# Performance work log

Measured on AMD Instinct MI355X. Metric: run time of the kernel, lower is better.

The kernel has to match this reference:

```python
import jax, jax.numpy as jnp
import numpy as np

B, S, DIM = 2, 2048, 2048
N_HEADS = 16
KV_LORA = 512
NOPE_D = 128
ROPE_D = 64
V_D = 128
Q_D = NOPE_D + ROPE_D  # 192
EPS = 1e-6


def _make_rope_cache(seqlen, head_dim):
    # [cos | sin] layout per position, GPT-NeoX half-rotation convention
    half = head_dim // 2
    inv_freq = 1.0 / (10000.0 ** (np.arange(0, half, dtype=np.float32) / half))
    t = np.arange(seqlen, dtype=np.float32)
    freqs = np.outer(t, inv_freq)                    # [S, half]
    emb = np.concatenate([freqs, freqs], axis=-1)    # [S, head_dim]
    return jnp.asarray(np.concatenate([np.cos(emb), np.sin(emb)], axis=-1))  # [S, 2*head_dim]


def setup_inputs() -> dict:
    key = jax.random.key(0)
    ks = jax.random.split(key, 6)
    x = jax.random.normal(ks[0], (B, S, DIM), dtype=jnp.float32)
    rope_cache = _make_rope_cache(S, ROPE_D)         # [S, 128]
    std = 0.02
    wq = jax.random.normal(ks[1], (N_HEADS * Q_D, DIM), dtype=jnp.float32) * std
    wkva = jax.random.normal(ks[2], (KV_LORA + ROPE_D, DIM), dtype=jnp.float32) * std
    norm_w = jnp.ones((KV_LORA,), dtype=jnp.float32)
    wkvb = jax.random.normal(ks[3], (N_HEADS * (NOPE_D + V_D), KV_LORA), dtype=jnp.float32) * std
    wo = jax.random.normal(ks[4], (DIM, N_HEADS * V_D), dtype=jnp.float32) * std
    return {"x": x, "rope_cache": rope_cache, "wq": wq, "wkva": wkva,
            "norm_w": norm_w, "wkvb": wkvb, "wo": wo}


def _rotate_half(t):
    h = t.shape[-1] // 2
    return jnp.concatenate([-t[..., h:], t[..., :h]], axis=-1)


def _rms_norm(t, w):
    tf = t.astype(jnp.float32)
    y = tf * jax.lax.rsqrt(jnp.mean(tf * tf, axis=-1, keepdims=True) + EPS)
    return (y * w).astype(t.dtype)


def reference(x, rope_cache, wq, wkva, norm_w, wkvb, wo):
    bs, seqlen, _ = x.shape
    scale = Q_D ** (-0.5)

    q = (x @ wq.T).reshape(bs, seqlen, N_HEADS, Q_D)
    q_nope, q_rope = q[..., :NOPE_D], q[..., NOPE_D:]

    ckv = x @ wkva.T                                 # [b,s,KV_LORA+ROPE_D]
    kv_pass, k_rope = ckv[..., :KV_LORA], ckv[..., KV_LORA:]
    kv = (_rms_norm(kv_pass, norm_w) @ wkvb.T).reshape(bs, seqlen, N_HEADS, NOPE_D + V_D)
    k_nope, v = kv[..., :NOPE_D], kv[..., NOPE_D:]

    k_rope = jnp.broadcast_to(k_rope[:, :, None, :], (bs, seqlen, N_HEADS, ROPE_D))

    cos = rope_cache[:seqlen, :ROPE_D][None, :, None, :]
    sin = rope_cache[:seqlen, ROPE_D:2 * ROPE_D][None, :, None, :]
    q_rope = q_rope * cos + _rotate_half(q_rope) * sin
    k_rope = k_rope * cos + _rotate_half(k_rope) * sin

    qf = jnp.concatenate([q_nope, q_rope], axis=-1)  # [b,s,h,192]
    kf = jnp.concatenate([k_nope, k_rope], axis=-1)

    # causal SDPA
    scores = jnp.einsum('bqhd,bkhd->bhqk', qf, kf) * scale
    mask = jnp.tril(jnp.ones((seqlen, seqlen), dtype=bool))
    scores = jnp.where(mask, scores, jnp.finfo(scores.dtype).min)
    probs = jax.nn.softmax(scores, axis=-1)
    out = jnp.einsum('bhqk,bkhd->bqhd', probs, v).reshape(bs, seqlen, N_HEADS * V_D)
    return out @ wo.T
```

## Files before the change

### kernel.cpp

```cpp
#include <hip/hip_runtime.h>
#include <cstdint>
#include <cstddef>

#define B_      2
#define S_      2048
#define DIM_    2048
#define H_      16
#define KV_LORA_ 512
#define NOPE_D_ 128
#define ROPE_D_ 64
#define V_D_    128
#define Q_D_    192
#define EPS_    1e-6f
#define BS_     (B_ * S_)
#define CKV_P_  768

typedef __attribute__((ext_vector_type(8))) short bf16x8;
typedef __attribute__((ext_vector_type(4))) float f32x4;
typedef __attribute__((ext_vector_type(16))) float f32x16;

__device__ __forceinline__ ushort f2bf(float f) {
    union { float f; uint32_t u; } v; v.f = f;
    uint32_t u = v.u + 0x7fff + ((v.u >> 16) & 1);
    return (ushort)(u >> 16);
}
__device__ __forceinline__ float bf2f(ushort u) {
    union { uint32_t u; float f; } v; v.u = (uint32_t)u << 16; return v.f;
}
__device__ __forceinline__ void gll16(const void* g, void* l) {
    __builtin_amdgcn_global_load_lds(
        (const __attribute__((address_space(1))) unsigned int*)g,
        (__attribute__((address_space(3))) unsigned int*)l, 16, 0, 0);
}

#define GQ_BARRIER()  __builtin_amdgcn_s_barrier()
#define GQ_LGKM0()    do { asm volatile("s_waitcnt lgkmcnt(0)" ::: "memory"); \
                           __builtin_amdgcn_sched_barrier(0); } while (0)

template <int MODE>
__global__ __launch_bounds__(512, 2) void gemm256_8ph(
    const ushort* __restrict__ A, const ushort* __restrict__ Bw,
    void* __restrict__ Cv, void* __restrict__ Cv2, int N, int K, int nbx)
{
    __shared__ __align__(16) ushort L[2][2][2][8192];

    const int tid = threadIdx.x;
    const int lane = tid & 63;
    const int w = tid >> 6;
    const int l15 = lane & 15, quad = lane >> 4;
    const int q8 = quad * 8;
    const int rsw8 = ((l15 >> 1) & 3) * 8;

    const int nwg = (int)gridDim.x;
    const int cpx = nwg >> 3;
    const int lin = (int)blockIdx.x;
    const int swz = (lin & 7) * cpx + (lin >> 3);
    const int m0 = (swz / nbx) * 256;
    const int n0 = (swz % nbx) * 256;

    const int wm0 = (w & 3) * 64;
    const int wn0 = (w >> 2) * 128;

    const int NT = K >> 6;

    f32x4 acc[4][8];
#pragma unroll
    for (int i = 0; i < 4; ++i)
#pragma unroll
        for (int j = 0; j < 8; ++j) acc[i][j] = (f32x4){0.f, 0.f, 0.f, 0.f};

    const int srow = lane >> 2;
    const int scg  = (lane & 3) ^ ((lane >> 3) & 3);

    auto stage = [&](int ab, int kh, int kt, int buf) {
#pragma unroll
        for (int j = 0; j < 2; ++j) {
            int ci = w + j * 8;
            ushort* dst = &L[buf][ab][kh][ci * 512 + lane * 8];
            int row = ci * 16 + srow;
            const ushort* src = (ab ? Bw + (size_t)(n0 + row) * K
                                    : A  + (size_t)(m0 + row) * K)
                                + kt * 64 + kh * 32 + scg * 8;
            gll16(src, dst);
        }
    };

    stage(0, 0, 0, 0); stage(1, 0, 0, 0); stage(0, 1, 0, 0); stage(1, 1, 0, 0);
    if (NT > 1) { stage(0, 0, 1, 1); stage(1, 0, 1, 1); stage(0, 1, 1, 1); }
    else        { stage(0, 0, 0, 1); stage(1, 0, 0, 1); stage(0, 1, 0, 1); }
    asm volatile("s_waitcnt vmcnt(6)" ::: "memory");
    GQ_BARRIER();

    bf16x8 a[4], b[4];

    for (int t = 0; t < NT; ++t) {
        const int c = t & 1, o = c ^ 1;
        const int kt1 = (t + 1 < NT) ? t + 1 : 0;
        const int kt2 = (t + 2 < NT) ? t + 2 : 0;

#pragma unroll
        for (int fm = 0; fm < 4; ++fm)
            a[fm] = *(const bf16x8*)&L[c][0][0][(wm0 + fm * 16 + l15) * 32 + (q8 ^ rsw8)];
#pragma unroll
        for (int fn = 0; fn < 4; ++fn)
            b[fn] = *(const bf16x8*)&L[c][1][0][(wn0 + fn * 16 + l15) * 32 + (q8 ^ rsw8)];
        stage(1, 1, kt1, o);
        GQ_BARRIER();
        GQ_LGKM0();
        __builtin_amdgcn_s_setprio(1);
#pragma unroll
        for (int fm = 0; fm < 4; ++fm)
#pragma unroll
            for (int fn = 0; fn < 4; ++fn)
                acc[fm][fn] = __builtin_amdgcn_mfma_f32_16x16x32_bf16(a[fm], b[fn], acc[fm][fn], 0, 0, 0);
        __builtin_amdgcn_s_setprio(0);
        GQ_BARRIER();

#pragma unroll
        for (int fn = 0; fn < 4; ++fn)
            b[fn] = *(const bf16x8*)&L[c][1][0][(wn0 + 64 + fn * 16 + l15) * 32 + (q8 ^ rsw8)];
        stage(0, 0, kt2, c);
        GQ_BARRIER();
        GQ_LGKM0();
        __builtin_amdgcn_s_setprio(1);
#pragma unroll
        for (int fm = 0; fm < 4; ++fm)
#pragma unroll
            for (int fn = 0; fn < 4; ++fn)
                acc[fm][4 + fn] = __builtin_amdgcn_mfma_f32_16x16x32_bf16(a[fm], b[fn], acc[fm][4 + fn], 0, 0, 0);
        __builtin_amdgcn_s_setprio(0);
        GQ_BARRIER();

#pragma unroll
        for (int fm = 0; fm < 4; ++fm)
            a[fm] = *(const bf16x8*)&L[c][0][1][(wm0 + fm * 16 + l15) * 32 + (q8 ^ rsw8)];
#pragma unroll
        for (int fn = 0; fn < 4; ++fn)
            b[fn] = *(const bf16x8*)&L[c][1][1][(wn0 + fn * 16 + l15) * 32 + (q8 ^ rsw8)];
        stage(1, 0, kt2, c);
        GQ_BARRIER();
        GQ_LGKM0();
        __builtin_amdgcn_s_setprio(1);
#pragma unroll
        for (int fm = 0; fm < 4; ++fm)
#pragma unroll
            for (int fn = 0; fn < 4; ++fn)
                acc[fm][fn] = __builtin_amdgcn_mfma_f32_16x16x32_bf16(a[fm], b[fn], acc[fm][fn], 0, 0, 0);
        __builtin_amdgcn_s_setprio(0);
        GQ_BARRIER();

#pragma unroll
        for (int fn = 0; fn < 4; ++fn)
            b[fn] = *(const bf16x8*)&L[c][1][1][(wn0 + 64 + fn * 16 + l15) * 32 + (q8 ^ rsw8)];
        stage(0, 1, kt2, c);
        GQ_BARRIER();
        GQ_LGKM0();
        __builtin_amdgcn_s_setprio(1);
#pragma unroll
        for (int fm = 0; fm < 4; ++fm)
#pragma unroll
            for (int fn = 0; fn < 4; ++fn)
                acc[fm][4 + fn] = __builtin_amdgcn_mfma_f32_16x16x32_bf16(a[fm], b[fn], acc[fm][4 + fn], 0, 0, 0);
        __builtin_amdgcn_s_setprio(0);
        asm volatile("s_waitcnt vmcnt(6)" ::: "memory");
        GQ_BARRIER();
    }

    if (MODE == 3) {
        asm volatile("s_waitcnt vmcnt(0)" ::: "memory");
        GQ_BARRIER();
        const int h = n0 >> 8;
        if (w < 4) {
#pragma unroll
            for (int fm = 0; fm < 4; ++fm)
#pragma unroll
                for (int r = 0; r < 4; ++r) {
                    size_t base = (size_t)(m0 + wm0 + fm * 16 + quad * 4 + r) * 4096
                                  + n0 + wn0 + l15;
#pragma unroll
                    for (int fn = 0; fn < 8; ++fn)
                        ((ushort*)Cv)[base + fn * 16] = f2bf(acc[fm][fn][r]);
                }
        } else {
            ushort* T = &L[0][0][0][0] + (size_t)(w - 4) * (128 * 80);
#pragma unroll
            for (int fm = 0; fm < 4; ++fm)
#pragma unroll
                for (int fn = 0; fn < 8; ++fn) {
                    uint32_t lo = (uint32_t)f2bf(acc[fm][fn][0])
                                | ((uint32_t)f2bf(acc[fm][fn][1]) << 16);
                    uint32_t hi2 = (uint32_t)f2bf(acc[fm][fn][2])
                                 | ((uint32_t)f2bf(acc[fm][fn][3]) << 16);
                    uint2 pk; pk.x = lo; pk.y = hi2;
                    *(uint2*)&T[(size_t)(fn * 16 + l15) * 80 + fm * 16 + quad * 4] = pk;
                }
            asm volatile("s_waitcnt lgkmcnt(0)" ::: "memory");
            __builtin_amdgcn_sched_barrier(0);
            const int bh = (m0 >> 11) * 16 + h;
            const int sbase = (m0 & 2047) + (w & 3) * 64;
            ushort* vT = (ushort*)Cv2;
#pragma unroll
            for (int j = 0; j < 16; ++j) {
                int cc = j * 64 + lane;
                int vd = cc >> 3;
                int s8 = (cc & 7) * 8;
                bf16x8 v = *(const bf16x8*)&T[(size_t)vd * 80 + s8];
                *(bf16x8*)(vT + ((size_t)bh * 128 + vd) * 2048 + sbase + s8) = v;
            }
        }
        return;
    }
#pragma unroll
    for (int fm = 0; fm < 4; ++fm)
#pragma unroll
        for (int r = 0; r < 4; ++r) {
            int row = m0 + wm0 + fm * 16 + quad * 4 + r;
            if (MODE == 2) {
                if (n0 < 3072) {
                    size_t base = (size_t)row * 3072 + n0 + wn0 + l15;
#pragma unroll
                    for (int fn = 0; fn < 8; ++fn)
                        ((ushort*)Cv)[base + fn * 16] = f2bf(acc[fm][fn][r]);
                } else {
                    size_t base = (size_t)row * CKV_P_ + (n0 - 3072) + wn0 + l15;
#pragma unroll
                    for (int fn = 0; fn < 8; ++fn)
                        ((float*)Cv2)[base + fn * 16] = acc[fm][fn][r];
                }
            } else {
                size_t base = (size_t)row * N + n0 + wn0 + l15;
#pragma unroll
                for (int fn = 0; fn < 8; ++fn) {
                    float v = acc[fm][fn][r];
                    if (MODE == 1) ((ushort*)Cv)[base + fn * 16] = f2bf(v);
                    else           ((float*)Cv)[base + fn * 16] = v;
                }
            }
        }
}

template <int OUT_BF16>
__global__ __launch_bounds__(512, 2) void gemm_bn128(
    const ushort* __restrict__ A, const ushort* __restrict__ Bw,
    void* __restrict__ Cv, int N, int K, int nbx)
{
    __shared__ __align__(16) ushort LA[2][2][8192];
    __shared__ __align__(16) ushort LB[2][2][4096];

    const int tid = threadIdx.x;
    const int lane = tid & 63;
    const int w = tid >> 6;
    const int l15 = lane & 15, quad = lane >> 4;
    const int q8 = quad * 8;
    const int rsw8 = ((l15 >> 1) & 3) * 8;

    const int nwg = (int)gridDim.x;
    const int cpx = nwg >> 3;
    const int lin = (int)blockIdx.x;
    const int swz = (lin & 7) * cpx + (lin >> 3);
    const int m0 = (swz / nbx) * 256;
    const int n0 = (swz % nbx) * 128;

    const int wm0 = (w & 3) * 64;
    const int wn0 = (w >> 2) * 64;

    const int NT = K >> 6;

    f32x4 acc[4][4];
#pragma unroll
    for (int i = 0; i < 4; ++i)
#pragma unroll
        for (int j = 0; j < 4; ++j) acc[i][j] = (f32x4){0.f, 0.f, 0.f, 0.f};

    const int srow = lane >> 2;
    const int scg  = (lane & 3) ^ ((lane >> 3) & 3);

    auto stageA = [&](int kh, int kt, int buf) {
#pragma unroll
        for (int j = 0; j < 2; ++j) {
            int ci = w + j * 8;
            ushort* dst = &LA[buf][kh][ci * 512 + lane * 8];
            int row = ci * 16 + srow;
            const ushort* src = A + (size_t)(m0 + row) * K
                                + kt * 64 + kh * 32 + scg * 8;
            gll16(src, dst);
        }
    };
    auto stageB = [&](int kt, int buf) {
#pragma unroll
        for (int j = 0; j < 2; ++j) {
            ushort* dst = &LB[buf][j][(w * 64 + lane) * 8];
            int row = w * 16 + srow;
            const ushort* src = Bw + (size_t)(n0 + row) * K
                                + kt * 64 + j * 32 + scg * 8;
            gll16(src, dst);
        }
    };

    stageA(0, 0, 0); stageA(1, 0, 0); stageB(0, 0);
    stageA(0, (NT > 1) ? 1 : 0, 1);
    asm volatile("s_waitcnt vmcnt(2)" ::: "memory");
    GQ_BARRIER();

    bf16x8 a[4], b[4];

    for (int t = 0; t < NT; ++t) {
        const int c = t & 1, o = c ^ 1;
        const int kt1 = (t + 1 < NT) ? t + 1 : 0;
        const int kt2 = (t + 2 < NT) ? t + 2 : 0;

#pragma unroll
        for (int fm = 0; fm < 4; ++fm)
            a[fm] = *(const bf16x8*)&LA[c][0][(wm0 + fm * 16 + l15) * 32 + (q8 ^ rsw8)];
#pragma unroll
        for (int fn = 0; fn < 4; ++fn)
            b[fn] = *(const bf16x8*)&LB[c][0][(wn0 + fn * 16 + l15) * 32 + (q8 ^ rsw8)];
        stageA(1, kt1, o); stageB(kt1, o);
        GQ_BARRIER();
        GQ_LGKM0();
        __builtin_amdgcn_s_setprio(1);
#pragma unroll
        for (int fm = 0; fm < 4; ++fm)
#pragma unroll
            for (int fn = 0; fn < 4; ++fn)
                acc[fm][fn] = __builtin_amdgcn_mfma_f32_16x16x32_bf16(a[fm], b[fn], acc[fm][fn], 0, 0, 0);
        __builtin_amdgcn_s_setprio(0);
        GQ_BARRIER();

#pragma unroll
        for (int fm = 0; fm < 4; ++fm)
            a[fm] = *(const bf16x8*)&LA[c][1][(wm0 + fm * 16 + l15) * 32 + (q8 ^ rsw8)];
#pragma unroll
        for (int fn = 0; fn < 4; ++fn)
            b[fn] = *(const bf16x8*)&LB[c][1][(wn0 + fn * 16 + l15) * 32 + (q8 ^ rsw8)];
        stageA(0, kt2, c);
        GQ_BARRIER();
        GQ_LGKM0();
        __builtin_amdgcn_s_setprio(1);
#pragma unroll
        for (int fm = 0; fm < 4; ++fm)
#pragma unroll
            for (int fn = 0; fn < 4; ++fn)
                acc[fm][fn] = __builtin_amdgcn_mfma_f32_16x16x32_bf16(a[fm], b[fn], acc[fm][fn], 0, 0, 0);
        __builtin_amdgcn_s_setprio(0);
        asm volatile("s_waitcnt vmcnt(2)" ::: "memory");
        GQ_BARRIER();
    }

#pragma unroll
    for (int fm = 0; fm < 4; ++fm)
#pragma unroll
        for (int r = 0; r < 4; ++r) {
            size_t base = (size_t)(m0 + wm0 + fm * 16 + quad * 4 + r) * N + n0 + wn0 + l15;
#pragma unroll
            for (int fn = 0; fn < 4; ++fn) {
                float v = acc[fm][fn][r];
                if (OUT_BF16) ((ushort*)Cv)[base + fn * 16] = f2bf(v);
                else          ((float*)Cv)[base + fn * 16] = v;
            }
        }
}

__global__ __launch_bounds__(256) void cast_all(
    const float* __restrict__ x, const float* __restrict__ wq,
    const float* __restrict__ wkva, const float* __restrict__ wkvb,
    const float* __restrict__ wo,
    ushort* __restrict__ xb, ushort* __restrict__ wc,
    ushort* __restrict__ wkvb_bf, ushort* __restrict__ wo_bf)
{
    size_t i = ((size_t)blockIdx.x * 256 + threadIdx.x) * 8;
    const float* s; ushort* d;
    if (i < 8388608)        { s = x + i;                  d = xb + i; }
    else if (i < 14680064)  { s = wq + (i - 8388608);     d = wc + (i - 8388608); }
    else if (i < 15859712)  { s = wkva + (i - 14680064);  d = wc + (i - 8388608); }
    else if (i < 16252928)  {
        ushort4 z = {0, 0, 0, 0};
        ushort* dz = wc + (i - 8388608);
        *(ushort4*)dz = z; *(ushort4*)(dz + 4) = z;
        return;
    }
    else if (i < 18350080)  { s = wkvb + (i - 16252928);  d = wkvb_bf + (i - 16252928); }
    else                    { s = wo + (i - 18350080);    d = wo_bf + (i - 18350080); }
    float4 a = *(const float4*)s;
    float4 b = *(const float4*)(s + 4);
    ushort4 o0, o1;
    o0.x = f2bf(a.x); o0.y = f2bf(a.y); o0.z = f2bf(a.z); o0.w = f2bf(a.w);
    o1.x = f2bf(b.x); o1.y = f2bf(b.y); o1.z = f2bf(b.z); o1.w = f2bf(b.w);
    *(ushort4*)d = o0;
    *(ushort4*)(d + 4) = o1;
}

__global__ __launch_bounds__(256) void rmsnorm_rope_k(
    const float* __restrict__ ckv, const float* __restrict__ nw,
    const float* __restrict__ rope_cache,
    ushort* __restrict__ cnorm, ushort* __restrict__ krb)
{
    const int lane = threadIdx.x & 63;
    const int row = blockIdx.x * 4 + (threadIdx.x >> 6);
    const float* src = ckv + (size_t)row * CKV_P_;
    float4 a = *(const float4*)(src + lane * 4);
    float4 b = *(const float4*)(src + 256 + lane * 4);
    float ss = a.x*a.x + a.y*a.y + a.z*a.z + a.w*a.w
             + b.x*b.x + b.y*b.y + b.z*b.z + b.w*b.w;
#pragma unroll
    for (int off = 32; off > 0; off >>= 1) ss += __shfl_xor(ss, off, 64);
    float rs = rsqrtf(ss * (1.0f / 512.0f) + EPS_);
    float4 w0 = *(const float4*)(nw + lane * 4);
    float4 w1 = *(const float4*)(nw + 256 + lane * 4);
    ushort* dst = cnorm + (size_t)row * KV_LORA_;
    ushort4 o0, o1;
    o0.x = f2bf(a.x*rs*w0.x); o0.y = f2bf(a.y*rs*w0.y);
    o0.z = f2bf(a.z*rs*w0.z); o0.w = f2bf(a.w*rs*w0.w);
    o1.x = f2bf(b.x*rs*w1.x); o1.y = f2bf(b.y*rs*w1.y);
    o1.z = f2bf(b.z*rs*w1.z); o1.w = f2bf(b.w*rs*w1.w);
    *(ushort4*)(dst + lane * 4) = o0;
    *(ushort4*)(dst + 256 + lane * 4) = o1;

    float v = src[KV_LORA_ + lane];
    float other = __shfl_xor(v, 32, 64);
    float rot = (lane < 32) ? -other : other;
    int s = row & (S_ - 1);
    float c  = rope_cache[s * (2 * ROPE_D_) + lane];
    float sn = rope_cache[s * (2 * ROPE_D_) + ROPE_D_ + lane];
    krb[(size_t)row * ROPE_D_ + lane] = f2bf(v * c + rot * sn);
}

__global__ __launch_bounds__(512, 2) void mla_attn_mfma7(
    const ushort* __restrict__ qb, const ushort* __restrict__ kvb,
    const ushort* __restrict__ krb, const ushort* __restrict__ vT,
    const float* __restrict__ rope_cache, ushort* __restrict__ attn)
{
    __shared__ __align__(16) ushort LDSU[40960];
    const int KNo[2] = {0, 8192};
    const int KRo[2] = {16384, 20480};
    const int VVo[2] = {24576, 32768};

    const int tid = threadIdx.x;
    const int lane = tid & 63;
    const int w = tid >> 6;
    const int l31 = lane & 31, hi = lane >> 5;
    const int band = w & 3;
    const int koff = (w >> 2) * 32;

    const int lin = (int)blockIdx.y * 8 + (int)blockIdx.x;
    const int swz = (lin & 7) * 32 + (lin >> 3);
    const int bh = swz >> 3;
    const int px = swz & 7;
    const int b = bh >> 4, h = bh & 15;
    const size_t bS = (size_t)b * S_;
    const float scale = 0.07216878364870323f;

    auto stage = [&](int kbase, int bufi) {
#pragma unroll
        for (int j = 0; j < 2; ++j) {
            int g = (j * 8 + w) * 64 + lane;
            int row = g >> 4;
            int d8 = (g & 15) ^ (row & 7);
            ushort* dst = &LDSU[KNo[bufi] + g * 8];
            const ushort* src = kvb + (bS + kbase + row) * 4096 + h * 256 + d8 * 8;
            gll16(src, dst);
        }
        {
            int g = w * 64 + lane;
            int row = g >> 3;
            int r8 = (g & 7) ^ (row & 7);
            ushort* dst = &LDSU[KRo[bufi] + g * 8];
            const ushort* src = krb + (bS + kbase + row) * 64 + r8 * 8;
            gll16(src, dst);
        }
#pragma unroll
        for (int j = 0; j < 2; ++j) {
            int g = (j * 8 + w) * 64 + lane;
            int vd = g >> 3;
            int kc = (g & 7) ^ (vd & 7);
            ushort* dst = &LDSU[VVo[bufi] + g * 8];
            const ushort* src = vT + ((size_t)bh * 128 + vd) * 2048 + kbase + kc * 8;
            gll16(src, dst);
        }
    };

#pragma unroll 1
    for (int hv = 0; hv < 2; ++hv) {
        const int qt = hv ? 15 - px : px;
        const int qbase = qt * 128;
        const int nkt = 2 * qt + 2;
        const int bmin = qbase + band * 32;

        stage(0, 0);

        bf16x8 qf[12];
        {
            const ushort* qrow = qb + (bS + bmin + l31) * (size_t)(H_ * Q_D_) + h * Q_D_;
#pragma unroll
            for (int c = 0; c < 8; ++c)
                qf[c] = *(const bf16x8*)(qrow + c * 16 + hi * 8);
            bf16x8 q8  = *(const bf16x8*)(qrow + 128 + hi * 8);
            bf16x8 q9  = *(const bf16x8*)(qrow + 144 + hi * 8);
            bf16x8 q10 = *(const bf16x8*)(qrow + 160 + hi * 8);
            bf16x8 q11 = *(const bf16x8*)(qrow + 176 + hi * 8);
            const float* rc = rope_cache + (size_t)(bmin + l31) * 128 + hi * 8;
            f32x4 c8a = *(const f32x4*)(rc + 0),  c8b = *(const f32x4*)(rc + 4);
            f32x4 c9a = *(const f32x4*)(rc + 16), c9b = *(const f32x4*)(rc + 20);
            f32x4 cAa = *(const f32x4*)(rc + 32), cAb = *(const f32x4*)(rc + 36);
            f32x4 cBa = *(const f32x4*)(rc + 48), cBb = *(const f32x4*)(rc + 52);
            f32x4 s8a = *(const f32x4*)(rc + 64), s8b = *(const f32x4*)(rc + 68);
            f32x4 s9a = *(const f32x4*)(rc + 80), s9b = *(const f32x4*)(rc + 84);
            f32x4 sAa = *(const f32x4*)(rc + 96), sAb = *(const f32x4*)(rc + 100);
            f32x4 sBa = *(const f32x4*)(rc + 112), sBb = *(const f32x4*)(rc + 116);
            bf16x8 o8, o9, o10, o11;
#pragma unroll
            for (int e = 0; e < 4; ++e) {
                float a8 = bf2f((ushort)q8[e]),  b8 = bf2f((ushort)q8[e + 4]);
                float a9 = bf2f((ushort)q9[e]),  b9 = bf2f((ushort)q9[e + 4]);
                float aA = bf2f((ushort)q10[e]), bA = bf2f((ushort)q10[e + 4]);
                float aB = bf2f((ushort)q11[e]), bB = bf2f((ushort)q11[e + 4]);
                o8[e]      = (short)f2bf(a8 * c8a[e] - aA * s8a[e]);
                o8[e + 4]  = (short)f2bf(b8 * c8b[e] - bA * s8b[e]);
                o9[e]      = (short)f2bf(a9 * c9a[e] - aB * s9a[e]);
                o9[e + 4]  = (short)f2bf(b9 * c9b[e] - bB * s9b[e]);
                o10[e]     = (short)f2bf(aA * cAa[e] + a8 * sAa[e]);
                o10[e + 4] = (short)f2bf(bA * cAb[e] + b8 * sAb[e]);
                o11[e]     = (short)f2bf(aB * cBa[e] + a9 * sBa[e]);
                o11[e + 4] = (short)f2bf(bB * cBb[e] + b9 * sBb[e]);
            }
            qf[8] = o8; qf[9] = o9; qf[10] = o10; qf[11] = o11;
        }

        f32x16 ov[4];
#pragma unroll
        for (int vt = 0; vt < 4; ++vt)
#pragma unroll
            for (int r = 0; r < 16; ++r) ov[vt][r] = 0.f;
        float m_run = -3e38f, lsum = 0.f;

        __syncthreads();

        const int krow = koff + l31;
        const int kx7 = krow & 7;
        const int vx7 = l31 & 7;

        for (int kt = 0; kt < nkt; ++kt) {
            const int kb = kt * 64;
            const int cur = kt & 1;
            if (kt + 1 < nkt) stage((kt + 1) * 64, cur ^ 1);

            const int kg = kb + koff;
            if (kg <= bmin + 31) {
                f32x16 sc;
#pragma unroll
                for (int r = 0; r < 16; ++r) sc[r] = 0.f;
                __builtin_amdgcn_s_setprio(1);
#pragma unroll
                for (int c = 0; c < 12; ++c) {
                    const bf16x8* kp;
                    if (c < 8)
                        kp = (const bf16x8*)&LDSU[KNo[cur] + (krow * 16 + ((c * 2 + hi) ^ kx7)) * 8];
                    else
                        kp = (const bf16x8*)&LDSU[KRo[cur] + (krow * 8 + (((c - 8) * 2 + hi) ^ kx7)) * 8];
                    sc = __builtin_amdgcn_mfma_f32_32x32x16_bf16(*kp, qf[c], sc, 0, 0, 0);
                }
                __builtin_amdgcn_s_setprio(0);

                const bool need_mask = (kg == bmin);
                float p[16]; float mx = -3e38f;
#pragma unroll
                for (int r = 0; r < 16; ++r) {
                    float v = sc[r] * scale;
                    if (need_mask) {
                        int kr = (r & 3) + 8 * (r >> 2) + 4 * hi;
                        if (kr > l31) v = -3e38f;
                    }
                    p[r] = v; mx = fmaxf(mx, v);
                }
                mx = fmaxf(mx, __shfl_xor(mx, 32, 64));
                if (!__all(mx - m_run <= 8.0f)) {
                    float mn = fmaxf(mx, m_run);
                    float al = __expf(m_run - mn);
                    m_run = mn; lsum *= al;
#pragma unroll
                    for (int vt = 0; vt < 4; ++vt)
#pragma unroll
                        for (int r = 0; r < 16; ++r) ov[vt][r] *= al;
                }
                float s_loc = 0.f;
#pragma unroll
                for (int r = 0; r < 16; ++r) { p[r] = __expf(p[r] - m_run); s_loc += p[r]; }
                lsum += s_loc + __shfl_xor(s_loc, 32, 64);

                uint32_t w8[8];
#pragma unroll
                for (int m = 0; m < 8; ++m)
                    w8[m] = (uint32_t)f2bf(p[2 * m]) | ((uint32_t)f2bf(p[2 * m + 1]) << 16);
                bf16x8 pb[2];
#pragma unroll
                for (int c = 0; c < 2; ++c) {
                    uint32_t wd[4];
#pragma unroll
                    for (int par = 0; par < 2; ++par) {
                        uint32_t a  = w8[4 * c + par];
                        uint32_t bb = w8[4 * c + 2 + par];
                        uint32_t t  = __shfl_xor(bb, 32, 64);
                        uint32_t t2 = __shfl_xor(a, 32, 64);
                        wd[par]     = hi ? t : a;
                        wd[par + 2] = hi ? bb : t2;
                    }
                    union { uint32_t u[4]; bf16x8 v; } cvt;
                    cvt.u[0] = wd[0]; cvt.u[1] = wd[1]; cvt.u[2] = wd[2]; cvt.u[3] = wd[3];
                    pb[c] = cvt.v;
                }

                __builtin_amdgcn_s_setprio(1);
#pragma unroll
                for (int vt = 0; vt < 4; ++vt)
#pragma unroll
                    for (int cc = 0; cc < 2; ++cc) {
                        int vd = vt * 32 + l31;
                        int k8 = (koff >> 3) + cc * 2 + hi;
                        bf16x8 vf = *(const bf16x8*)
                            &LDSU[VVo[cur] + (vd * 8 + (k8 ^ vx7)) * 8];
                        ov[vt] = __builtin_amdgcn_mfma_f32_32x32x16_bf16(vf, pb[cc], ov[vt], 0, 0, 0);
                    }
                __builtin_amdgcn_s_setprio(0);
            }
            __syncthreads();
        }

        float* mrg = (float*)LDSU;
        if (w >= 4) {
            float* dst = mrg + (size_t)((w - 4) * 64 + lane) * 68;
#pragma unroll
            for (int vt = 0; vt < 4; ++vt)
#pragma unroll
                for (int g = 0; g < 4; ++g) {
                    f32x4 v4v = { ov[vt][g * 4 + 0], ov[vt][g * 4 + 1],
                                  ov[vt][g * 4 + 2], ov[vt][g * 4 + 3] };
                    *(f32x4*)(dst + vt * 16 + g * 4) = v4v;
                }
            dst[64] = m_run; dst[65] = lsum;
        }
        __syncthreads();
        if (w < 4) {
            const float* srcm = mrg + (size_t)(w * 64 + lane) * 68;
            float mB = srcm[64], lB = srcm[65];
            float M = fmaxf(m_run, mB);
            float eA = __expf(m_run - M), eB = __expf(mB - M);
            float L = lsum * eA + lB * eB;
            float inv = 1.0f / L;
            size_t obase = (bS + bmin + l31) * (size_t)(H_ * V_D_) + h * V_D_;
#pragma unroll
            for (int vt = 0; vt < 4; ++vt)
#pragma unroll
                for (int g = 0; g < 4; ++g) {
                    ushort4 o;
                    o.x = f2bf((ov[vt][g*4+0] * eA + srcm[vt*16+g*4+0] * eB) * inv);
                    o.y = f2bf((ov[vt][g*4+1] * eA + srcm[vt*16+g*4+1] * eB) * inv);
                    o.z = f2bf((ov[vt][g*4+2] * eA + srcm[vt*16+g*4+2] * eB) * inv);
                    o.w = f2bf((ov[vt][g*4+3] * eA + srcm[vt*16+g*4+3] * eB) * inv);
                    *(ushort4*)(attn + obase + vt * 32 + g * 8 + hi * 4) = o;
                }
        }
        __syncthreads();
    }
}

extern "C" void kernel_launch(void* const* d_in, const int* in_sizes, int n_in,
                              void* d_out, int out_size, void* d_ws, size_t ws_size,
                              hipStream_t stream)
{
    const float* x          = (const float*)d_in[0];
    const float* rope_cache = (const float*)d_in[1];
    const float* wq         = (const float*)d_in[2];
    const float* wkva       = (const float*)d_in[3];
    const float* norm_w     = (const float*)d_in[4];
    const float* wkvb       = (const float*)d_in[5];
    const float* wo         = (const float*)d_in[6];
    float* out = (float*)d_out;

    char* p = (char*)d_ws;
    ushort* xb       = (ushort*)p; p += (size_t)BS_ * DIM_ * 2;
    ushort* q_bf     = (ushort*)p; p += (size_t)BS_ * H_ * Q_D_ * 2;
    float*  ckv      = (float*) p; p += (size_t)BS_ * CKV_P_ * 4;
    ushort* cnorm_bf = (ushort*)p; p += (size_t)BS_ * KV_LORA_ * 2;
    ushort* kvb      = (ushort*)p; p += (size_t)BS_ * 4096 * 2;
    ushort* attn_bf  = (ushort*)p; p += (size_t)BS_ * 2048 * 2;
    ushort* krb      = (ushort*)p; p += (size_t)BS_ * ROPE_D_ * 2;
    ushort* wc_bf    = (ushort*)p; p += (size_t)3840 * DIM_ * 2;
    ushort* wkvb_bf  = (ushort*)p; p += (size_t)4096 * KV_LORA_ * 2;
    ushort* wo_bf    = (ushort*)p; p += (size_t)DIM_ * 2048 * 2;
    ushort* vT       = xb;

    cast_all<<<11008, dim3(256), 0, stream>>>(
        x, wq, wkva, wkvb, wo, xb, wc_bf, wkvb_bf, wo_bf);

    gemm256_8ph<2><<<dim3(16 * 15), dim3(512), 0, stream>>>(
        xb, wc_bf, q_bf, ckv, 0, DIM_, 15);
    rmsnorm_rope_k<<<BS_ / 4, dim3(256), 0, stream>>>(
        ckv, norm_w, rope_cache, cnorm_bf, krb);
    gemm256_8ph<3><<<dim3(16 * 16), dim3(512), 0, stream>>>(
        cnorm_bf, wkvb_bf, kvb, vT, 4096, KV_LORA_, 16);
    mla_attn_mfma7<<<dim3(8, B_ * H_), dim3(512), 0, stream>>>(
        q_bf, kvb, krb, vT, rope_cache, attn_bf);
    gemm_bn128<0><<<dim3(16 * 16), dim3(512), 0, stream>>>(
        attn_bf, wo_bf, out, 2048, 2048, 16);
}
```

Before: 340.7 us.

## Split attention into one q-tile per block with XCD-aware mapping and exp2 softmax

```diff
diff --git a/kernel.cpp b/kernel.cpp
--- a/kernel.cpp
+++ b/kernel.cpp
@@ -425,7 +425,7 @@
     krb[(size_t)row * ROPE_D_ + lane] = f2bf(v * c + rot * sn);
 }
 
-__global__ __launch_bounds__(512, 2) void mla_attn_mfma7(
+__global__ __launch_bounds__(512, 4) void mla_attn_mfma8(
     const ushort* __restrict__ qb, const ushort* __restrict__ kvb,
     const ushort* __restrict__ krb, const ushort* __restrict__ vT,
     const float* __restrict__ rope_cache, ushort* __restrict__ attn)
@@ -442,13 +442,15 @@
     const int band = w & 3;
     const int koff = (w >> 2) * 32;
 
-    const int lin = (int)blockIdx.y * 8 + (int)blockIdx.x;
-    const int swz = (lin & 7) * 32 + (lin >> 3);
-    const int bh = swz >> 3;
-    const int px = swz & 7;
+    const int lin = (int)blockIdx.x;
+    const int r256 = lin & 255, sl = lin >> 8;
+    const int xcd = r256 & 7, cu = r256 >> 3;
+    const int bh = xcd * 4 + (cu >> 3);
+    const int jj = cu & 7;
+    const int qt = sl ? (15 - jj) : jj;
     const int b = bh >> 4, h = bh & 15;
     const size_t bS = (size_t)b * S_;
-    const float scale = 0.07216878364870323f;
+    const float sc_l2e = 0.10411789f;
 
     auto stage = [&](int kbase, int bufi) {
 #pragma unroll
@@ -479,187 +481,190 @@
         }
     };
 
-#pragma unroll 1
-    for (int hv = 0; hv < 2; ++hv) {
-        const int qt = hv ? 15 - px : px;
-        const int qbase = qt * 128;
-        const int nkt = 2 * qt + 2;
-        const int bmin = qbase + band * 32;
-
-        stage(0, 0);
-
-        bf16x8 qf[12];
-        {
-            const ushort* qrow = qb + (bS + bmin + l31) * (size_t)(H_ * Q_D_) + h * Q_D_;
-#pragma unroll
-            for (int c = 0; c < 8; ++c)
-                qf[c] = *(const bf16x8*)(qrow + c * 16 + hi * 8);
-            bf16x8 q8  = *(const bf16x8*)(qrow + 128 + hi * 8);
-            bf16x8 q9  = *(const bf16x8*)(qrow + 144 + hi * 8);
-            bf16x8 q10 = *(const bf16x8*)(qrow + 160 + hi * 8);
-            bf16x8 q11 = *(const bf16x8*)(qrow + 176 + hi * 8);
-            const float* rc = rope_cache + (size_t)(bmin + l31) * 128 + hi * 8;
-            f32x4 c8a = *(const f32x4*)(rc + 0),  c8b = *(const f32x4*)(rc + 4);
-            f32x4 c9a = *(const f32x4*)(rc + 16), c9b = *(const f32x4*)(rc + 20);
-            f32x4 cAa = *(const f32x4*)(rc + 32), cAb = *(const f32x4*)(rc + 36);
-            f32x4 cBa = *(const f32x4*)(rc + 48), cBb = *(const f32x4*)(rc + 52);
-            f32x4 s8a = *(const f32x4*)(rc + 64), s8b = *(const f32x4*)(rc + 68);
-            f32x4 s9a = *(const f32x4*)(rc + 80), s9b = *(const f32x4*)(rc + 84);
-            f32x4 sAa = *(const f32x4*)(rc + 96), sAb = *(const f32x4*)(rc + 100);
-            f32x4 sBa = *(const f32x4*)(rc + 112), sBb = *(const f32x4*)(rc + 116);
-            bf16x8 o8, o9, o10, o11;
-#pragma unroll
-            for (int e = 0; e < 4; ++e) {
-                float a8 = bf2f((ushort)q8[e]),  b8 = bf2f((ushort)q8[e + 4]);
-                float a9 = bf2f((ushort)q9[e]),  b9 = bf2f((ushort)q9[e + 4]);
-                float aA = bf2f((ushort)q10[e]), bA = bf2f((ushort)q10[e + 4]);
-                float aB = bf2f((ushort)q11[e]), bB = bf2f((ushort)q11[e + 4]);
-                o8[e]      = (short)f2bf(a8 * c8a[e] - aA * s8a[e]);
-                o8[e + 4]  = (short)f2bf(b8 * c8b[e] - bA * s8b[e]);
-                o9[e]      = (short)f2bf(a9 * c9a[e] - aB * s9a[e]);
-                o9[e + 4]  = (short)f2bf(b9 * c9b[e] - bB * s9b[e]);
-                o10[e]     = (short)f2bf(aA * cAa[e] + a8 * sAa[e]);
-                o10[e + 4] = (short)f2bf(bA * cAb[e] + b8 * sAb[e]);
-                o11[e]     = (short)f2bf(aB * cBa[e] + a9 * sBa[e]);
-                o11[e + 4] = (short)f2bf(bB * cBb[e] + b9 * sBb[e]);
-            }
-            qf[8] = o8; qf[9] = o9; qf[10] = o10; qf[11] = o11;
-        }
-
-        f32x16 ov[4];
+    const int qbase = qt * 128;
+    const int nkt = 2 * qt + 2;
+    const int bmin = qbase + band * 32;
+
+    stage(0, 0);
+
+    bf16x8 qf[12];
+    {
+        const ushort* qrow = qb + (bS + bmin + l31) * (size_t)(H_ * Q_D_) + h * Q_D_;
+#pragma unroll
+        for (int c = 0; c < 8; ++c)
+            qf[c] = *(const bf16x8*)(qrow + c * 16 + hi * 8);
+        bf16x8 q8  = *(const bf16x8*)(qrow + 128 + hi * 8);
+        bf16x8 q9  = *(const bf16x8*)(qrow + 144 + hi * 8);
+        bf16x8 q10 = *(const bf16x8*)(qrow + 160 + hi * 8);
+        bf16x8 q11 = *(const bf16x8*)(qrow + 176 + hi * 8);
+        const float* rc = rope_cache + (size_t)(bmin + l31) * 128 + hi * 8;
+        f32x4 c8a = *(const f32x4*)(rc + 0),  c8b = *(const f32x4*)(rc + 4);
+        f32x4 c9a = *(const f32x4*)(rc + 16), c9b = *(const f32x4*)(rc + 20);
+        f32x4 cAa = *(const f32x4*)(rc + 32), cAb = *(const f32x4*)(rc + 36);
+        f32x4 cBa = *(const f32x4*)(rc + 48), cBb = *(const f32x4*)(rc + 52);
+        f32x4 s8a = *(const f32x4*)(rc + 64), s8b = *(const f32x4*)(rc + 68);
+        f32x4 s9a = *(const f32x4*)(rc + 80), s9b = *(const f32x4*)(rc + 84);
+        f32x4 sAa = *(const f32x4*)(rc + 96), sAb = *(const f32x4*)(rc + 100);
+        f32x4 sBa = *(const f32x4*)(rc + 112), sBb = *(const f32x4*)(rc + 116);
+        bf16x8 o8, o9, o10, o11;
+#pragma unroll
+        for (int e = 0; e < 4; ++e) {
+            float a8 = bf2f((ushort)q8[e]),  b8 = bf2f((ushort)q8[e + 4]);
+            float a9 = bf2f((ushort)q9[e]),  b9 = bf2f((ushort)q9[e + 4]);
+            float aA = bf2f((ushort)q10[e]), bA = bf2f((ushort)q10[e + 4]);
+            float aB = bf2f((ushort)q11[e]), bB = bf2f((ushort)q11[e + 4]);
+            o8[e]      = (short)f2bf(a8 * c8a[e] - aA * s8a[e]);
+            o8[e + 4]  = (short)f2bf(b8 * c8b[e] - bA * s8b[e]);
+            o9[e]      = (short)f2bf(a9 * c9a[e] - aB * s9a[e]);
+            o9[e + 4]  = (short)f2bf(b9 * c9b[e] - bB * s9b[e]);
+            o10[e]     = (short)f2bf(aA * cAa[e] + a8 * sAa[e]);
+            o10[e + 4] = (short)f2bf(bA * cAb[e] + b8 * sAb[e]);
+            o11[e]     = (short)f2bf(aB * cBa[e] + a9 * sBa[e]);
+            o11[e + 4] = (short)f2bf(bB * cBb[e] + b9 * sBb[e]);
+        }
+        qf[8] = o8; qf[9] = o9; qf[10] = o10; qf[11] = o11;
+    }
+
+    f32x16 ov[4];
+#pragma unroll
+    for (int vt = 0; vt < 4; ++vt)
+#pragma unroll
+        for (int r = 0; r < 16; ++r) ov[vt][r] = 0.f;
+    float m_run = -3e38f, lsum = 0.f;
+
+    __syncthreads();
+
+    const int krow = koff + l31;
+    const int kx7 = krow & 7;
+    const int vx7 = l31 & 7;
+
+    for (int kt = 0; kt < nkt; ++kt) {
+        const int kb = kt * 64;
+        const int cur = kt & 1;
+        if (kt + 1 < nkt) stage((kt + 1) * 64, cur ^ 1);
+
+        const int kg = kb + koff;
+        if (kg <= bmin + 31) {
+            f32x16 sc;
+#pragma unroll
+            for (int r = 0; r < 16; ++r) sc[r] = 0.f;
+            __builtin_amdgcn_s_setprio(1);
+#pragma unroll
+            for (int c = 0; c < 12; ++c) {
+                const bf16x8* kp;
+                if (c < 8)
+                    kp = (const bf16x8*)&LDSU[KNo[cur] + (krow * 16 + ((c * 2 + hi) ^ kx7)) * 8];
+                else
+                    kp = (const bf16x8*)&LDSU[KRo[cur] + (krow * 8 + (((c - 8) * 2 + hi) ^ kx7)) * 8];
+                sc = __builtin_amdgcn_mfma_f32_32x32x16_bf16(*kp, qf[c], sc, 0, 0, 0);
+            }
+            __builtin_amdgcn_s_setprio(0);
+
+            const bool need_mask = (kg == bmin);
+            float p[16]; float mx = -3e38f;
+#pragma unroll
+            for (int r = 0; r < 16; ++r) {
+                float v = sc[r] * sc_l2e;
+                if (need_mask) {
+                    int kr = (r & 3) + 8 * (r >> 2) + 4 * hi;
+                    if (kr > l31) v = -3e38f;
+                }
+                p[r] = v; mx = fmaxf(mx, v);
+            }
+            mx = fmaxf(mx, __shfl_xor(mx, 32, 64));
+            if (!__all(mx - m_run <= 11.5416f)) {
+                float mn = fmaxf(mx, m_run);
+                float al;
+                asm("v_exp_f32 %0, %1" : "=v"(al) : "v"(m_run - mn));
+                m_run = mn; lsum *= al;
+#pragma unroll
+                for (int vt = 0; vt < 4; ++vt)
+#pragma unroll
+                    for (int r = 0; r < 16; ++r) ov[vt][r] *= al;
+            }
+            float s_loc = 0.f;
+#pragma unroll
+            for (int r = 0; r < 16; ++r) {
+                float e;
+                asm("v_exp_f32 %0, %1" : "=v"(e) : "v"(p[r] - m_run));
+                p[r] = e; s_loc += e;
+            }
+            lsum += s_loc + __shfl_xor(s_loc, 32, 64);
+
+            uint32_t w8[8];
+#pragma unroll
+            for (int m = 0; m < 8; ++m)
+                asm("v_cvt_pk_bf16_f32 %0, %1, %2"
+                    : "=v"(w8[m]) : "v"(p[2 * m]), "v"(p[2 * m + 1]));
+            bf16x8 pb[2];
+#pragma unroll
+            for (int c = 0; c < 2; ++c) {
+                uint32_t wd[4];
+#pragma unroll
+                for (int par = 0; par < 2; ++par) {
+                    uint32_t a  = w8[4 * c + par];
+                    uint32_t bb = w8[4 * c + 2 + par];
+                    uint32_t t  = __shfl_xor(bb, 32, 64);
+                    uint32_t t2 = __shfl_xor(a, 32, 64);
+                    wd[par]     = hi ? t : a;
+                    wd[par + 2] = hi ? bb : t2;
+                }
+                union { uint32_t u[4]; bf16x8 v; } cvt;
+                cvt.u[0] = wd[0]; cvt.u[1] = wd[1]; cvt.u[2] = wd[2]; cvt.u[3] = wd[3];
+                pb[c] = cvt.v;
+            }
+
+            __builtin_amdgcn_s_setprio(1);
+#pragma unroll
+            for (int vt = 0; vt < 4; ++vt)
+#pragma unroll
+                for (int cc = 0; cc < 2; ++cc) {
+                    int vd = vt * 32 + l31;
+                    int k8 = (koff >> 3) + cc * 2 + hi;
+                    bf16x8 vf = *(const bf16x8*)
+                        &LDSU[VVo[cur] + (vd * 8 + (k8 ^ vx7)) * 8];
+                    ov[vt] = __builtin_amdgcn_mfma_f32_32x32x16_bf16(vf, pb[cc], ov[vt], 0, 0, 0);
+                }
+            __builtin_amdgcn_s_setprio(0);
+        }
+        __syncthreads();
+    }
+
+    float* mrg = (float*)LDSU;
+    if (w >= 4) {
+        float* dst = mrg + (size_t)((w - 4) * 64 + lane) * 68;
 #pragma unroll
         for (int vt = 0; vt < 4; ++vt)
 #pragma unroll
-            for (int r = 0; r < 16; ++r) ov[vt][r] = 0.f;
-        float m_run = -3e38f, lsum = 0.f;
-
-        __syncthreads();
-
-        const int krow = koff + l31;
-        const int kx7 = krow & 7;
-        const int vx7 = l31 & 7;
-
-        for (int kt = 0; kt < nkt; ++kt) {
-            const int kb = kt * 64;
-            const int cur = kt & 1;
-            if (kt + 1 < nkt) stage((kt + 1) * 64, cur ^ 1);
-
-            const int kg = kb + koff;
-            if (kg <= bmin + 31) {
-                f32x16 sc;
-#pragma unroll
-                for (int r = 0; r < 16; ++r) sc[r] = 0.f;
-                __builtin_amdgcn_s_setprio(1);
-#pragma unroll
-                for (int c = 0; c < 12; ++c) {
-                    const bf16x8* kp;
-                    if (c < 8)
-                        kp = (const bf16x8*)&LDSU[KNo[cur] + (krow * 16 + ((c * 2 + hi) ^ kx7)) * 8];
-                    else
-                        kp = (const bf16x8*)&LDSU[KRo[cur] + (krow * 8 + (((c - 8) * 2 + hi) ^ kx7)) * 8];
-                    sc = __builtin_amdgcn_mfma_f32_32x32x16_bf16(*kp, qf[c], sc, 0, 0, 0);
-                }
-                __builtin_amdgcn_s_setprio(0);
-
-                const bool need_mask = (kg == bmin);
-                float p[16]; float mx = -3e38f;
-#pragma unroll
-                for (int r = 0; r < 16; ++r) {
-                    float v = sc[r] * scale;
-                    if (need_mask) {
-                        int kr = (r & 3) + 8 * (r >> 2) + 4 * hi;
-                        if (kr > l31) v = -3e38f;
-                    }
-                    p[r] = v; mx = fmaxf(mx, v);
-                }
-                mx = fmaxf(mx, __shfl_xor(mx, 32, 64));
-                if (!__all(mx - m_run <= 8.0f)) {
-                    float mn = fmaxf(mx, m_run);
-                    float al = __expf(m_run - mn);
-                    m_run = mn; lsum *= al;
-#pragma unroll
-                    for (int vt = 0; vt < 4; ++vt)
-#pragma unroll
-                        for (int r = 0; r < 16; ++r) ov[vt][r] *= al;
-                }
-                float s_loc = 0.f;
-#pragma unroll
-                for (int r = 0; r < 16; ++r) { p[r] = __expf(p[r] - m_run); s_loc += p[r]; }
-                lsum += s_loc + __shfl_xor(s_loc, 32, 64);
-
-                uint32_t w8[8];
-#pragma unroll
-                for (int m = 0; m < 8; ++m)
-                    w8[m] = (uint32_t)f2bf(p[2 * m]) | ((uint32_t)f2bf(p[2 * m + 1]) << 16);
-                bf16x8 pb[2];
-#pragma unroll
-                for (int c = 0; c < 2; ++c) {
-                    uint32_t wd[4];
-#pragma unroll
-                    for (int par = 0; par < 2; ++par) {
-                        uint32_t a  = w8[4 * c + par];
-                        uint32_t bb = w8[4 * c + 2 + par];
-                        uint32_t t  = __shfl_xor(bb, 32, 64);
-                        uint32_t t2 = __shfl_xor(a, 32, 64);
-                        wd[par]     = hi ? t : a;
-                        wd[par + 2] = hi ? bb : t2;
-                    }
-                    union { uint32_t u[4]; bf16x8 v; } cvt;
-                    cvt.u[0] = wd[0]; cvt.u[1] = wd[1]; cvt.u[2] = wd[2]; cvt.u[3] = wd[3];
-                    pb[c] = cvt.v;
-                }
-
-                __builtin_amdgcn_s_setprio(1);
-#pragma unroll
-                for (int vt = 0; vt < 4; ++vt)
-#pragma unroll
-                    for (int cc = 0; cc < 2; ++cc) {
-                        int vd = vt * 32 + l31;
-                        int k8 = (koff >> 3) + cc * 2 + hi;
-                        bf16x8 vf = *(const bf16x8*)
-                            &LDSU[VVo[cur] + (vd * 8 + (k8 ^ vx7)) * 8];
-                        ov[vt] = __builtin_amdgcn_mfma_f32_32x32x16_bf16(vf, pb[cc], ov[vt], 0, 0, 0);
-                    }
-                __builtin_amdgcn_s_setprio(0);
-            }
-            __syncthreads();
-        }
-
-        float* mrg = (float*)LDSU;
-        if (w >= 4) {
-            float* dst = mrg + (size_t)((w - 4) * 64 + lane) * 68;
-#pragma unroll
-            for (int vt = 0; vt < 4; ++vt)
-#pragma unroll
-                for (int g = 0; g < 4; ++g) {
-                    f32x4 v4v = { ov[vt][g * 4 + 0], ov[vt][g * 4 + 1],
-                                  ov[vt][g * 4 + 2], ov[vt][g * 4 + 3] };
-                    *(f32x4*)(dst + vt * 16 + g * 4) = v4v;
-                }
-            dst[64] = m_run; dst[65] = lsum;
-        }
-        __syncthreads();
-        if (w < 4) {
-            const float* srcm = mrg + (size_t)(w * 64 + lane) * 68;
-            float mB = srcm[64], lB = srcm[65];
-            float M = fmaxf(m_run, mB);
-            float eA = __expf(m_run - M), eB = __expf(mB - M);
-            float L = lsum * eA + lB * eB;
-            float inv = 1.0f / L;
-            size_t obase = (bS + bmin + l31) * (size_t)(H_ * V_D_) + h * V_D_;
-#pragma unroll
-            for (int vt = 0; vt < 4; ++vt)
-#pragma unroll
-                for (int g = 0; g < 4; ++g) {
-                    ushort4 o;
-                    o.x = f2bf((ov[vt][g*4+0] * eA + srcm[vt*16+g*4+0] * eB) * inv);
-                    o.y = f2bf((ov[vt][g*4+1] * eA + srcm[vt*16+g*4+1] * eB) * inv);
-                    o.z = f2bf((ov[vt][g*4+2] * eA + srcm[vt*16+g*4+2] * eB) * inv);
-                    o.w = f2bf((ov[vt][g*4+3] * eA + srcm[vt*16+g*4+3] * eB) * inv);
-                    *(ushort4*)(attn + obase + vt * 32 + g * 8 + hi * 4) = o;
-                }
-        }
-        __syncthreads();
+            for (int g = 0; g < 4; ++g) {
+                f32x4 v4v = { ov[vt][g * 4 + 0], ov[vt][g * 4 + 1],
+                              ov[vt][g * 4 + 2], ov[vt][g * 4 + 3] };
+                *(f32x4*)(dst + vt * 16 + g * 4) = v4v;
+            }
+        dst[64] = m_run; dst[65] = lsum;
+    }
+    __syncthreads();
+    if (w < 4) {
+        const float* srcm = mrg + (size_t)(w * 64 + lane) * 68;
+        float mB = srcm[64], lB = srcm[65];
+        float M = fmaxf(m_run, mB);
+        float eA, eB;
+        asm("v_exp_f32 %0, %1" : "=v"(eA) : "v"(m_run - M));
+        asm("v_exp_f32 %0, %1" : "=v"(eB) : "v"(mB - M));
+        float L = lsum * eA + lB * eB;
+        float inv = 1.0f / L;
+        size_t obase = (bS + bmin + l31) * (size_t)(H_ * V_D_) + h * V_D_;
+#pragma unroll
+        for (int vt = 0; vt < 4; ++vt)
+#pragma unroll
+            for (int g = 0; g < 4; ++g) {
+                ushort4 o;
+                o.x = f2bf((ov[vt][g*4+0] * eA + srcm[vt*16+g*4+0] * eB) * inv);
+                o.y = f2bf((ov[vt][g*4+1] * eA + srcm[vt*16+g*4+1] * eB) * inv);
+                o.z = f2bf((ov[vt][g*4+2] * eA + srcm[vt*16+g*4+2] * eB) * inv);
+                o.w = f2bf((ov[vt][g*4+3] * eA + srcm[vt*16+g*4+3] * eB) * inv);
+                *(ushort4*)(attn + obase + vt * 32 + g * 8 + hi * 4) = o;
+            }
     }
 }
 
@@ -698,7 +703,7 @@
         ckv, norm_w, rope_cache, cnorm_bf, krb);
     gemm256_8ph<3><<<dim3(16 * 16), dim3(512), 0, stream>>>(
         cnorm_bf, wkvb_bf, kvb, vT, 4096, KV_LORA_, 16);
-    mla_attn_mfma7<<<dim3(8, B_ * H_), dim3(512), 0, stream>>>(
+    mla_attn_mfma8<<<dim3(512), dim3(512), 0, stream>>>(
         q_bf, kvb, krb, vT, rope_cache, attn_bf);
     gemm_bn128<0><<<dim3(16 * 16), dim3(512), 0, stream>>>(
         attn_bf, wo_bf, out, 2048, 2048, 16);
```

Result: slower. 476.6 us (+39.9%).
